# Performance work log

Hardware: AMD Instinct MI355X
Metric: run time of the kernel (lower is better)

The kernel has to match this reference:

```python
import jax, jax.numpy as jnp
import numpy as np

N_NODES = 50000


def gcn_conv(x, W, b, src, dst, n_nodes):
    # PyG GCNConv: h = W x; out = D^{-1/2} (A + I) D^{-1/2} h + b
    h = x @ W  # [N, out_dim]
    ones = jnp.ones(src.shape[0], dtype=x.dtype)
    # degree with self-loops, counted on destination nodes
    deg = jax.ops.segment_sum(ones, dst, num_segments=n_nodes) + 1.0
    dinv = jax.lax.rsqrt(deg)  # deg >= 1, always safe
    norm = dinv[src] * dinv[dst]  # [E]
    agg = jax.ops.segment_sum(h[src] * norm[:, None], dst, num_segments=n_nodes)
    agg = agg + h * (dinv * dinv)[:, None]  # self-loop contribution
    return agg + b


def setup_inputs() -> dict:
    key = jax.random.key(0)
    k1, k2, k3, k4 = jax.random.split(key, 4)
    input_dim, hidden_dim, output_dim = 512, 256, 64
    n_edges = 1_600_000
    x = jax.random.normal(k1, (N_NODES, input_dim), dtype=jnp.float32)
    edge_index = jax.random.randint(k2, (2, n_edges), 0, N_NODES, dtype=jnp.int32)
    W1 = jax.random.normal(k3, (input_dim, hidden_dim), dtype=jnp.float32) / np.sqrt(input_dim)
    b1 = jnp.zeros((hidden_dim,), dtype=jnp.float32)
    W2 = jax.random.normal(k4, (hidden_dim, output_dim), dtype=jnp.float32) / np.sqrt(hidden_dim)
    b2 = jnp.zeros((output_dim,), dtype=jnp.float32)
    return {"x": x, "W1": W1, "b1": b1, "W2": W2, "b2": b2, "edge_index": edge_index}


def reference(x, W1, b1, W2, b2, edge_index):
    src, dst = edge_index[0], edge_index[1]
    h = jax.nn.relu(gcn_conv(x, W1, b1, src, dst, N_NODES))
    h = gcn_conv(h, W2, b2, src, dst, N_NODES)
    return jax.nn.log_softmax(h, axis=1)
```

## Files before the change

kernel.cpp:

```cpp
#include <hip/hip_runtime.h>

#define NODES 50000
#define NBIN 196
#define EPB 2048

typedef __attribute__((ext_vector_type(8))) short short8;
typedef __attribute__((ext_vector_type(4))) float f32x4;
typedef __attribute__((ext_vector_type(2))) float f32x2;

__device__ __forceinline__ ushort f2bf(float f) {
    uint u = __float_as_uint(f);
    uint r = (u + 0x7fffu + ((u >> 16) & 1u)) >> 16;
    return (ushort)r;
}
__device__ __forceinline__ float bf2f(ushort u) {
    return __uint_as_float(((uint)u) << 16);
}
__device__ __forceinline__ uchar f2fp8(float f) {
    return (uchar)(__builtin_amdgcn_cvt_pk_fp8_f32(f, f, 0, false) & 0xff);
}
__device__ __forceinline__ uint cvtpk_bf16(float lo, float hi) {
    uint r;
    asm("v_cvt_pk_bf16_f32 %0, %1, %2" : "=v"(r) : "v"(lo), "v"(hi));
    return r;
}


__global__ __launch_bounds__(256) void k_hist(const int* __restrict__ dst, int E,
                                              int* __restrict__ hist, int nblk) {
    __shared__ int h[NBIN];
    int t = threadIdx.x;
    for (int i = t; i < NBIN; i += 256) h[i] = 0;
    __syncthreads();
    int base = blockIdx.x * EPB;
#pragma unroll
    for (int i = 0; i < EPB / 256; ++i) {
        int e = base + i * 256 + t;
        if (e < E) atomicAdd(&h[dst[e] >> 8], 1);
    }
    __syncthreads();
    for (int i = t; i < NBIN; i += 256) hist[i * nblk + blockIdx.x] = h[i];
}

__global__ __launch_bounds__(1024) void k_scanbin(const int* __restrict__ hist,
                                                  int* __restrict__ offl,
                                                  int* __restrict__ btot, int nblk) {
    __shared__ int s[1024];
    int b = blockIdx.x, t = threadIdx.x;
    int v = (t < nblk) ? hist[b * nblk + t] : 0;
    s[t] = v;
    __syncthreads();
    for (int off = 1; off < 1024; off <<= 1) {
        int u = (t >= off) ? s[t - off] : 0;
        __syncthreads();
        s[t] += u;
        __syncthreads();
    }
    if (t < nblk) offl[b * nblk + t] = s[t] - v;
    if (t == 1023) btot[b] = s[1023];
}

__global__ __launch_bounds__(256) void k_scanoff(const int* __restrict__ btot,
                                                 int* __restrict__ binoff,
                                                 int* __restrict__ rowstart, int E) {
    __shared__ int s[256];
    int t = threadIdx.x;
    int v = (t < NBIN) ? btot[t] : 0;
    s[t] = v;
    __syncthreads();
    for (int off = 1; off < 256; off <<= 1) {
        int u = (t >= off) ? s[t - off] : 0;
        __syncthreads();
        s[t] += u;
        __syncthreads();
    }
    if (t < NBIN) binoff[t] = s[t] - v;
    if (t == 0) { binoff[NBIN] = E; rowstart[NODES] = E; }
}

__global__ __launch_bounds__(256) void k_part(const int* __restrict__ src,
                                              const int* __restrict__ dst, int E,
                                              const int* __restrict__ offl,
                                              const int* __restrict__ binoff, int nblk,
                                              int2* __restrict__ tmp) {
    __shared__ int cur[NBIN];
    int t = threadIdx.x, blk = blockIdx.x;
    for (int i = t; i < NBIN; i += 256) cur[i] = binoff[i] + offl[i * nblk + blk];
    __syncthreads();
    int base = blk * EPB;
#pragma unroll
    for (int i = 0; i < EPB / 256; ++i) {
        int e = base + i * 256 + t;
        if (e < E) {
            int d = dst[e];
            int p = atomicAdd(&cur[d >> 8], 1);
            tmp[p] = make_int2(src[e], d);
        }
    }
}

__global__ __launch_bounds__(256) void k_csr(const int2* __restrict__ tmp,
                                             const int* __restrict__ binoff,
                                             int* __restrict__ rowstart,
                                             float* __restrict__ dinv,
                                             int* __restrict__ esrc) {
    __shared__ int ncnt[256], nst[256];
    int b = blockIdx.x, t = threadIdx.x;
    int e0 = binoff[b], e1 = binoff[b + 1];
    int nb0 = b << 8;
    int nn = min(256, NODES - nb0);
    ncnt[t] = 0;
    __syncthreads();
    for (int e = e0 + t; e < e1; e += 256) atomicAdd(&ncnt[tmp[e].y - nb0], 1);
    __syncthreads();
    int v = ncnt[t];
    nst[t] = v;
    __syncthreads();
    for (int off = 1; off < 256; off <<= 1) {
        int u = (t >= off) ? nst[t - off] : 0;
        __syncthreads();
        nst[t] += u;
        __syncthreads();
    }
    int excl = nst[t] - v;
    if (t < nn) {
        rowstart[nb0 + t] = e0 + excl;
        dinv[nb0 + t] = rsqrtf(1.0f + (float)v);
    }
    __syncthreads();
    ncnt[t] = e0 + excl;
    __syncthreads();
    for (int e = e0 + t; e < e1; e += 256) {
        int2 q = tmp[e];
        int p = atomicAdd(&ncnt[q.y - nb0], 1);
        esrc[p] = q.x;
    }
}

__global__ void k_wfill(const int* __restrict__ esrc, const float* __restrict__ dinv,
                        float* __restrict__ ew, int E) {
    int e = blockIdx.x * blockDim.x + threadIdx.x;
    if (e < E) ew[e] = dinv[esrc[e]];
}


__global__ void k_castT(const float* __restrict__ in, ushort* __restrict__ out, int R, int C) {
    int i = blockIdx.x * blockDim.x + threadIdx.x;
    if (i >= R * C) return;
    int r = i / C, c = i % C;
    out[(size_t)c * R + r] = f2bf(in[i]);
}

__global__ __launch_bounds__(256) void k_gemm1(const float* __restrict__ x,
                                               const ushort* __restrict__ w1t,
                                               uchar* __restrict__ h1f8, int M, int K) {
    constexpr int BM = 64, BN = 128, BK = 64;
    __shared__ __align__(16) ushort As[BM * BK];
    __shared__ __align__(16) ushort Bs[BN * BK];

    int t = threadIdx.x;
    int w = t >> 6, l = t & 63;
    int wm = w & 1, wn = w >> 1;
    int bm = blockIdx.x * BM, bn = blockIdx.y * BN;
    int lr = l & 15, g4 = l >> 4;

    f32x4 acc[2][4] = {};

    int ar = t >> 2;
    int aq = t & 3;
    int arow_g = bm + ar;
    bool aok = arow_g < M;
    const float* ap = x + (size_t)arow_g * K + aq * 16;
    char* adst = (char*)As + ar * 128;
    int aswz = (ar & 7) << 4;

    int brow_loc = l >> 3;
    int bseg = ((l & 7) << 4) ^ (brow_loc << 4);

    for (int k0 = 0; k0 < K; k0 += BK) {
#pragma unroll
        for (int i = 0; i < 4; ++i) {
            int rbase = w * 32 + i * 8;
            const char* gsrc = (const char*)w1t + (size_t)(bn + rbase + brow_loc) * (K * 2) + k0 * 2 + bseg;
            __builtin_amdgcn_global_load_lds(
                (const __attribute__((address_space(1))) uint*)gsrc,
                (__attribute__((address_space(3))) uint*)((char*)Bs + rbase * 128),
                16, 0, 0);
        }
        {
            float4 f[4];
#pragma unroll
            for (int j = 0; j < 4; ++j)
                f[j] = aok ? *(const float4*)(ap + k0 + j * 4) : make_float4(0.f, 0.f, 0.f, 0.f);
#pragma unroll
            for (int j = 0; j < 2; ++j) {
                uint p0 = cvtpk_bf16(f[2 * j].x, f[2 * j].y);
                uint p1 = cvtpk_bf16(f[2 * j].z, f[2 * j].w);
                uint p2 = cvtpk_bf16(f[2 * j + 1].x, f[2 * j + 1].y);
                uint p3 = cvtpk_bf16(f[2 * j + 1].z, f[2 * j + 1].w);
                int4 v = make_int4((int)p0, (int)p1, (int)p2, (int)p3);
                *(int4*)(adst + ((aq * 32 + j * 16) ^ aswz)) = v;
            }
        }
        __syncthreads();
#pragma unroll
        for (int ks = 0; ks < 2; ++ks) {
            short8 af[2], bfr[4];
#pragma unroll
            for (int mt = 0; mt < 2; ++mt) {
                int r = wm * 32 + mt * 16 + lr;
                af[mt] = *(const short8*)((const char*)As + r * 128 + ((ks * 64 + g4 * 16) ^ ((r & 7) << 4)));
            }
#pragma unroll
            for (int nt = 0; nt < 4; ++nt) {
                int r = wn * 64 + nt * 16 + lr;
                bfr[nt] = *(const short8*)((const char*)Bs + r * 128 + ((ks * 64 + g4 * 16) ^ ((r & 7) << 4)));
            }
#pragma unroll
            for (int mt = 0; mt < 2; ++mt)
#pragma unroll
                for (int nt = 0; nt < 4; ++nt)
                    acc[mt][nt] = __builtin_amdgcn_mfma_f32_16x16x32_bf16(af[mt], bfr[nt], acc[mt][nt], 0, 0, 0);
        }
        __syncthreads();
    }

#pragma unroll
    for (int mt = 0; mt < 2; ++mt)
#pragma unroll
        for (int nt = 0; nt < 4; ++nt)
#pragma unroll
            for (int i = 0; i < 4; ++i) {
                int row = bm + wm * 32 + mt * 16 + g4 * 4 + i;
                int col = bn + wn * 64 + nt * 16 + lr;
                if (row < M) h1f8[(size_t)row * 256 + col] = f2fp8(acc[mt][nt][i]);
            }
}

__global__ __launch_bounds__(256) void k_gemm2(const ushort* __restrict__ A,
                                               const ushort* __restrict__ Bt,
                                               ushort* __restrict__ Cb,
                                               int M, int K) {
    constexpr int BM = 64, BN = 64;
    constexpr int NT = 4;
    constexpr int SA = 40;
    __shared__ ushort As[BM * SA];
    __shared__ ushort Bs[BN * SA];

    int t = threadIdx.x;
    int w = t >> 6, l = t & 63;
    int bm = blockIdx.x * BM;
    int lr = l & 15, lk = (l >> 4) * 8;

    f32x4 acc[NT] = {};
    const int ACH = BM * 4;
    const int BCH = BN * 4;

    for (int k0 = 0; k0 < K; k0 += 32) {
        for (int c = t; c < ACH + BCH; c += 256) {
            if (c < ACH) {
                int row = c >> 2, seg = c & 3;
                int gr = bm + row;
                int4 v = make_int4(0, 0, 0, 0);
                if (gr < M) v = *(const int4*)(A + (size_t)gr * K + k0 + seg * 8);
                *(int4*)(&As[row * SA + seg * 8]) = v;
            } else {
                int cc = c - ACH;
                int row = cc >> 2, seg = cc & 3;
                int4 v = *(const int4*)(Bt + (size_t)row * K + k0 + seg * 8);
                *(int4*)(&Bs[row * SA + seg * 8]) = v;
            }
        }
        __syncthreads();
        short8 af = *(const short8*)(&As[(w * 16 + lr) * SA + lk]);
        short8 bfr[NT];
#pragma unroll
        for (int nt = 0; nt < NT; ++nt)
            bfr[nt] = *(const short8*)(&Bs[(nt * 16 + lr) * SA + lk]);
#pragma unroll
        for (int nt = 0; nt < NT; ++nt)
            acc[nt] = __builtin_amdgcn_mfma_f32_16x16x32_bf16(af, bfr[nt], acc[nt], 0, 0, 0);
        __syncthreads();
    }

#pragma unroll
    for (int nt = 0; nt < NT; ++nt)
#pragma unroll
        for (int i = 0; i < 4; ++i) {
            int row = bm + w * 16 + (l >> 4) * 4 + i;
            int col = nt * 16 + lr;
            if (row < M) Cb[(size_t)row * BN + col] = f2bf(acc[nt][i]);
        }
}

__global__ __launch_bounds__(256) void k_agg1(const uchar* __restrict__ h8,
                                              const int* __restrict__ rowstart,
                                              const int* __restrict__ esrc,
                                              const float* __restrict__ ew,
                                              const float* __restrict__ dinv,
                                              const float* __restrict__ b1,
                                              ushort* __restrict__ out) {
    int wave = threadIdx.x >> 6;
    int lane = threadIdx.x & 63;
    int n = blockIdx.x * 4 + wave;
    if (n >= NODES) return;
    float4 acc = make_float4(0.f, 0.f, 0.f, 0.f);
    int e0 = rowstart[n], e1 = rowstart[n + 1];
    int e = e0;
#define A1_STEP(wt, qv)                                                       \
    {                                                                         \
        f32x2 lo = __builtin_amdgcn_cvt_pk_f32_fp8((int)(qv), false);         \
        f32x2 hi = __builtin_amdgcn_cvt_pk_f32_fp8((int)(qv), true);          \
        acc.x = fmaf(wt, lo[0], acc.x);                                       \
        acc.y = fmaf(wt, lo[1], acc.y);                                       \
        acc.z = fmaf(wt, hi[0], acc.z);                                       \
        acc.w = fmaf(wt, hi[1], acc.w);                                       \
    }
    for (; e + 8 <= e1; e += 8) {
        int s0 = esrc[e],     s1 = esrc[e + 1], s2 = esrc[e + 2], s3 = esrc[e + 3];
        int s4 = esrc[e + 4], s5 = esrc[e + 5], s6 = esrc[e + 6], s7 = esrc[e + 7];
        float w0 = ew[e],     w1 = ew[e + 1], w2 = ew[e + 2], w3 = ew[e + 3];
        float w4 = ew[e + 4], w5 = ew[e + 5], w6 = ew[e + 6], w7 = ew[e + 7];
        uint v0 = *(const uint*)(h8 + (size_t)s0 * 256 + lane * 4);
        uint v1 = *(const uint*)(h8 + (size_t)s1 * 256 + lane * 4);
        uint v2 = *(const uint*)(h8 + (size_t)s2 * 256 + lane * 4);
        uint v3 = *(const uint*)(h8 + (size_t)s3 * 256 + lane * 4);
        uint v4 = *(const uint*)(h8 + (size_t)s4 * 256 + lane * 4);
        uint v5 = *(const uint*)(h8 + (size_t)s5 * 256 + lane * 4);
        uint v6 = *(const uint*)(h8 + (size_t)s6 * 256 + lane * 4);
        uint v7 = *(const uint*)(h8 + (size_t)s7 * 256 + lane * 4);
        A1_STEP(w0, v0) A1_STEP(w1, v1) A1_STEP(w2, v2) A1_STEP(w3, v3)
        A1_STEP(w4, v4) A1_STEP(w5, v5) A1_STEP(w6, v6) A1_STEP(w7, v7)
    }
    for (; e < e1; ++e) {
        int s = esrc[e];
        float wt = ew[e];
        uint v = *(const uint*)(h8 + (size_t)s * 256 + lane * 4);
        A1_STEP(wt, v)
    }
#undef A1_STEP
    float dn = dinv[n];
    float s2v = dn * dn;
    uint qs = *(const uint*)(h8 + (size_t)n * 256 + lane * 4);
    f32x2 slo = __builtin_amdgcn_cvt_pk_f32_fp8((int)qs, false);
    f32x2 shi = __builtin_amdgcn_cvt_pk_f32_fp8((int)qs, true);
    float4 bb = *(const float4*)(b1 + lane * 4);
    ushort4 r;
    r.x = f2bf(fmaxf(fmaf(acc.x, dn, fmaf(slo[0], s2v, bb.x)), 0.f));
    r.y = f2bf(fmaxf(fmaf(acc.y, dn, fmaf(slo[1], s2v, bb.y)), 0.f));
    r.z = f2bf(fmaxf(fmaf(acc.z, dn, fmaf(shi[0], s2v, bb.z)), 0.f));
    r.w = f2bf(fmaxf(fmaf(acc.w, dn, fmaf(shi[1], s2v, bb.w)), 0.f));
    *(ushort4*)(out + (size_t)n * 256 + lane * 4) = r;
}

__global__ __launch_bounds__(256) void k_agg2(const ushort* __restrict__ h,
                                              const int* __restrict__ rowstart,
                                              const int* __restrict__ esrc,
                                              const float* __restrict__ ew,
                                              const float* __restrict__ dinv,
                                              const float* __restrict__ b2,
                                              float* __restrict__ out) {
    int wave = threadIdx.x >> 6;
    int lane = threadIdx.x & 63;
    int n = blockIdx.x * 4 + wave;
    if (n >= NODES) return;
    float acc = 0.f;
    int e0 = rowstart[n], e1 = rowstart[n + 1];
    int e = e0;
    for (; e + 8 <= e1; e += 8) {
        int s0 = esrc[e],     s1 = esrc[e + 1], s2 = esrc[e + 2], s3 = esrc[e + 3];
        int s4 = esrc[e + 4], s5 = esrc[e + 5], s6 = esrc[e + 6], s7 = esrc[e + 7];
        float w0 = ew[e],     w1 = ew[e + 1], w2 = ew[e + 2], w3 = ew[e + 3];
        float w4 = ew[e + 4], w5 = ew[e + 5], w6 = ew[e + 6], w7 = ew[e + 7];
        float v0 = bf2f(h[(size_t)s0 * 64 + lane]);
        float v1 = bf2f(h[(size_t)s1 * 64 + lane]);
        float v2 = bf2f(h[(size_t)s2 * 64 + lane]);
        float v3 = bf2f(h[(size_t)s3 * 64 + lane]);
        float v4 = bf2f(h[(size_t)s4 * 64 + lane]);
        float v5 = bf2f(h[(size_t)s5 * 64 + lane]);
        float v6 = bf2f(h[(size_t)s6 * 64 + lane]);
        float v7 = bf2f(h[(size_t)s7 * 64 + lane]);
        acc = fmaf(w0, v0, acc); acc = fmaf(w1, v1, acc);
        acc = fmaf(w2, v2, acc); acc = fmaf(w3, v3, acc);
        acc = fmaf(w4, v4, acc); acc = fmaf(w5, v5, acc);
        acc = fmaf(w6, v6, acc); acc = fmaf(w7, v7, acc);
    }
    for (; e < e1; ++e)
        acc = fmaf(ew[e], bf2f(h[(size_t)esrc[e] * 64 + lane]), acc);
    float dn = dinv[n];
    float r = fmaf(acc, dn, fmaf(bf2f(h[(size_t)n * 64 + lane]), dn * dn, b2[lane]));
    float m = r;
#pragma unroll
    for (int off = 32; off; off >>= 1) m = fmaxf(m, __shfl_xor(m, off));
    float ex = __expf(r - m);
    float ssum = ex;
#pragma unroll
    for (int off = 32; off; off >>= 1) ssum += __shfl_xor(ssum, off);
    out[(size_t)n * 64 + lane] = r - m - __logf(ssum);
}


extern "C" void kernel_launch(void* const* d_in, const int* in_sizes, int n_in,
                              void* d_out, int out_size, void* d_ws, size_t ws_size,
                              hipStream_t stream) {
    const float* x  = (const float*)d_in[0];
    const float* W1 = (const float*)d_in[1];
    const float* b1 = (const float*)d_in[2];
    const float* W2 = (const float*)d_in[3];
    const float* b2 = (const float*)d_in[4];
    const int*   ei = (const int*)d_in[5];
    int E = in_sizes[5] / 2;
    const int* src = ei;
    const int* dst = ei + E;
    float* out = (float*)d_out;

    int nblk = (E + EPB - 1) / EPB;

    char* wsp = (char*)d_ws;
    auto alloc = [&](size_t bytes) {
        char* p = wsp;
        wsp += (bytes + 255) & ~(size_t)255;
        return p;
    };
    int*    hist     = (int*)alloc((size_t)NBIN * nblk * 4);
    int*    offl     = (int*)alloc((size_t)NBIN * nblk * 4);
    int*    btot     = (int*)alloc((size_t)NBIN * 4);
    int*    binoff   = (int*)alloc((size_t)(NBIN + 1) * 4);
    int*    rowstart = (int*)alloc((size_t)(NODES + 1) * 4);
    float*  dinv     = (float*)alloc((size_t)NODES * 4);
    int2*   tmp      = (int2*)alloc((size_t)E * 8);
    int*    esrc     = (int*)alloc((size_t)E * 4);
    float*  ew       = (float*)alloc((size_t)E * 4);
    ushort* w1t      = (ushort*)alloc((size_t)256 * 512 * 2);
    ushort* w2t      = (ushort*)alloc((size_t)64 * 256 * 2);
    uchar*  h1f8     = (uchar*)alloc((size_t)NODES * 256);
    ushort* h1ab     = (ushort*)alloc((size_t)NODES * 256 * 2);
    ushort* h2b      = (ushort*)alloc((size_t)NODES * 64 * 2);

    k_hist<<<nblk, 256, 0, stream>>>(dst, E, hist, nblk);
    k_scanbin<<<NBIN, 1024, 0, stream>>>(hist, offl, btot, nblk);
    k_scanoff<<<1, 256, 0, stream>>>(btot, binoff, rowstart, E);
    k_part<<<nblk, 256, 0, stream>>>(src, dst, E, offl, binoff, nblk, tmp);
    k_csr<<<NBIN, 256, 0, stream>>>(tmp, binoff, rowstart, dinv, esrc);
    k_wfill<<<(E + 255) / 256, 256, 0, stream>>>(esrc, dinv, ew, E);

    k_castT<<<(512 * 256 + 255) / 256, 256, 0, stream>>>(W1, w1t, 512, 256);
    k_castT<<<(256 * 64 + 255) / 256, 256, 0, stream>>>(W2, w2t, 256, 64);

    k_gemm1<<<dim3((NODES + 63) / 64, 2), 256, 0, stream>>>(x, w1t, h1f8, NODES, 512);
    k_agg1<<<(NODES + 3) / 4, 256, 0, stream>>>(h1f8, rowstart, esrc, ew, dinv, b1, h1ab);

    k_gemm2<<<(NODES + 63) / 64, 256, 0, stream>>>(h1ab, w2t, h2b, NODES, 256);
    k_agg2<<<(NODES + 3) / 4, 256, 0, stream>>>(h2b, rowstart, esrc, ew, dinv, b2, out);
}
```

Baseline: 226.3 us.

## Fuse edge partition into GEMM1 launch and scalarize aggregation row bounds

Merges the edge-partition kernel into the first GEMM launch as extra blocks in the same grid, so the memory-bound scatter can overlap with the compute-bound GEMM and one launch is removed. The GEMM grid is flattened to 1D, with the N tile taken from the low bit of the block index. In both aggregation kernels, the wave index and row bounds are forced into scalar registers via readfirstlane, and the per-lane base pointer is hoisted out of the loop. The fused kernel's shared-memory footprint covers both roles, which may slightly lower occupancy, and the partition blocks are scheduled after the GEMM blocks.

```diff
diff --git a/kernel.cpp b/kernel.cpp
--- a/kernel.cpp
+++ b/kernel.cpp
@@ -76,27 +76,6 @@
     }
     if (t < NBIN) binoff[t] = s[t] - v;
     if (t == 0) { binoff[NBIN] = E; rowstart[NODES] = E; }
-}
-
-__global__ __launch_bounds__(256) void k_part(const int* __restrict__ src,
-                                              const int* __restrict__ dst, int E,
-                                              const int* __restrict__ offl,
-                                              const int* __restrict__ binoff, int nblk,
-                                              int2* __restrict__ tmp) {
-    __shared__ int cur[NBIN];
-    int t = threadIdx.x, blk = blockIdx.x;
-    for (int i = t; i < NBIN; i += 256) cur[i] = binoff[i] + offl[i * nblk + blk];
-    __syncthreads();
-    int base = blk * EPB;
-#pragma unroll
-    for (int i = 0; i < EPB / 256; ++i) {
-        int e = base + i * 256 + t;
-        if (e < E) {
-            int d = dst[e];
-            int p = atomicAdd(&cur[d >> 8], 1);
-            tmp[p] = make_int2(src[e], d);
-        }
-    }
 }
 
 __global__ __launch_bounds__(256) void k_csr(const int2* __restrict__ tmp,
@@ -151,17 +130,40 @@
     out[(size_t)c * R + r] = f2bf(in[i]);
 }
 
-__global__ __launch_bounds__(256) void k_gemm1(const float* __restrict__ x,
-                                               const ushort* __restrict__ w1t,
-                                               uchar* __restrict__ h1f8, int M, int K) {
+__global__ __launch_bounds__(256) void k_gemm1_part(
+    const float* __restrict__ x, const ushort* __restrict__ w1t,
+    uchar* __restrict__ h1f8, int M, int K,
+    const int* __restrict__ src, const int* __restrict__ dst, int E,
+    const int* __restrict__ offl, const int* __restrict__ binoff, int nblk,
+    int2* __restrict__ tmp, int gemmBlocks) {
     constexpr int BM = 64, BN = 128, BK = 64;
     __shared__ __align__(16) ushort As[BM * BK];
     __shared__ __align__(16) ushort Bs[BN * BK];
+    __shared__ int cur[NBIN];
 
     int t = threadIdx.x;
+
+    if (blockIdx.x >= gemmBlocks) {
+        int blk = blockIdx.x - gemmBlocks;
+        for (int i = t; i < NBIN; i += 256) cur[i] = binoff[i] + offl[i * nblk + blk];
+        __syncthreads();
+        int base = blk * EPB;
+#pragma unroll
+        for (int i = 0; i < EPB / 256; ++i) {
+            int e = base + i * 256 + t;
+            if (e < E) {
+                int d = dst[e];
+                int p = atomicAdd(&cur[d >> 8], 1);
+                tmp[p] = make_int2(src[e], d);
+            }
+        }
+        return;
+    }
+
     int w = t >> 6, l = t & 63;
     int wm = w & 1, wn = w >> 1;
-    int bm = blockIdx.x * BM, bn = blockIdx.y * BN;
+    int bm = (blockIdx.x >> 1) * BM;
+    int bn = (blockIdx.x & 1) * BN;
     int lr = l & 15, g4 = l >> 4;
 
     f32x4 acc[2][4] = {};
@@ -300,12 +302,14 @@
                                               const float* __restrict__ dinv,
                                               const float* __restrict__ b1,
                                               ushort* __restrict__ out) {
-    int wave = threadIdx.x >> 6;
+    int wave = __builtin_amdgcn_readfirstlane(threadIdx.x >> 6);
     int lane = threadIdx.x & 63;
     int n = blockIdx.x * 4 + wave;
     if (n >= NODES) return;
+    const uchar* hl = h8 + lane * 4;
     float4 acc = make_float4(0.f, 0.f, 0.f, 0.f);
-    int e0 = rowstart[n], e1 = rowstart[n + 1];
+    int e0 = __builtin_amdgcn_readfirstlane(rowstart[n]);
+    int e1 = __builtin_amdgcn_readfirstlane(rowstart[n + 1]);
     int e = e0;
 #define A1_STEP(wt, qv)                                                       \
     {                                                                         \
@@ -321,27 +325,27 @@
         int s4 = esrc[e + 4], s5 = esrc[e + 5], s6 = esrc[e + 6], s7 = esrc[e + 7];
         float w0 = ew[e],     w1 = ew[e + 1], w2 = ew[e + 2], w3 = ew[e + 3];
         float w4 = ew[e + 4], w5 = ew[e + 5], w6 = ew[e + 6], w7 = ew[e + 7];
-        uint v0 = *(const uint*)(h8 + (size_t)s0 * 256 + lane * 4);
-        uint v1 = *(const uint*)(h8 + (size_t)s1 * 256 + lane * 4);
-        uint v2 = *(const uint*)(h8 + (size_t)s2 * 256 + lane * 4);
-        uint v3 = *(const uint*)(h8 + (size_t)s3 * 256 + lane * 4);
-        uint v4 = *(const uint*)(h8 + (size_t)s4 * 256 + lane * 4);
-        uint v5 = *(const uint*)(h8 + (size_t)s5 * 256 + lane * 4);
-        uint v6 = *(const uint*)(h8 + (size_t)s6 * 256 + lane * 4);
-        uint v7 = *(const uint*)(h8 + (size_t)s7 * 256 + lane * 4);
+        uint v0 = *(const uint*)(hl + (size_t)s0 * 256);
+        uint v1 = *(const uint*)(hl + (size_t)s1 * 256);
+        uint v2 = *(const uint*)(hl + (size_t)s2 * 256);
+        uint v3 = *(const uint*)(hl + (size_t)s3 * 256);
+        uint v4 = *(const uint*)(hl + (size_t)s4 * 256);
+        uint v5 = *(const uint*)(hl + (size_t)s5 * 256);
+        uint v6 = *(const uint*)(hl + (size_t)s6 * 256);
+        uint v7 = *(const uint*)(hl + (size_t)s7 * 256);
         A1_STEP(w0, v0) A1_STEP(w1, v1) A1_STEP(w2, v2) A1_STEP(w3, v3)
         A1_STEP(w4, v4) A1_STEP(w5, v5) A1_STEP(w6, v6) A1_STEP(w7, v7)
     }
     for (; e < e1; ++e) {
         int s = esrc[e];
         float wt = ew[e];
-        uint v = *(const uint*)(h8 + (size_t)s * 256 + lane * 4);
+        uint v = *(const uint*)(hl + (size_t)s * 256);
         A1_STEP(wt, v)
     }
 #undef A1_STEP
     float dn = dinv[n];
     float s2v = dn * dn;
-    uint qs = *(const uint*)(h8 + (size_t)n * 256 + lane * 4);
+    uint qs = *(const uint*)(hl + (size_t)n * 256);
     f32x2 slo = __builtin_amdgcn_cvt_pk_f32_fp8((int)qs, false);
     f32x2 shi = __builtin_amdgcn_cvt_pk_f32_fp8((int)qs, true);
     float4 bb = *(const float4*)(b1 + lane * 4);
@@ -360,35 +364,37 @@
                                               const float* __restrict__ dinv,
                                               const float* __restrict__ b2,
                                               float* __restrict__ out) {
-    int wave = threadIdx.x >> 6;
+    int wave = __builtin_amdgcn_readfirstlane(threadIdx.x >> 6);
     int lane = threadIdx.x & 63;
     int n = blockIdx.x * 4 + wave;
     if (n >= NODES) return;
+    const ushort* hl = h + lane;
     float acc = 0.f;
-    int e0 = rowstart[n], e1 = rowstart[n + 1];
+    int e0 = __builtin_amdgcn_readfirstlane(rowstart[n]);
+    int e1 = __builtin_amdgcn_readfirstlane(rowstart[n + 1]);
     int e = e0;
     for (; e + 8 <= e1; e += 8) {
         int s0 = esrc[e],     s1 = esrc[e + 1], s2 = esrc[e + 2], s3 = esrc[e + 3];
         int s4 = esrc[e + 4], s5 = esrc[e + 5], s6 = esrc[e + 6], s7 = esrc[e + 7];
         float w0 = ew[e],     w1 = ew[e + 1], w2 = ew[e + 2], w3 = ew[e + 3];
         float w4 = ew[e + 4], w5 = ew[e + 5], w6 = ew[e + 6], w7 = ew[e + 7];
-        float v0 = bf2f(h[(size_t)s0 * 64 + lane]);
-        float v1 = bf2f(h[(size_t)s1 * 64 + lane]);
-        float v2 = bf2f(h[(size_t)s2 * 64 + lane]);
-        float v3 = bf2f(h[(size_t)s3 * 64 + lane]);
-        float v4 = bf2f(h[(size_t)s4 * 64 + lane]);
-        float v5 = bf2f(h[(size_t)s5 * 64 + lane]);
-        float v6 = bf2f(h[(size_t)s6 * 64 + lane]);
-        float v7 = bf2f(h[(size_t)s7 * 64 + lane]);
+        float v0 = bf2f(hl[(size_t)s0 * 64]);
+        float v1 = bf2f(hl[(size_t)s1 * 64]);
+        float v2 = bf2f(hl[(size_t)s2 * 64]);
+        float v3 = bf2f(hl[(size_t)s3 * 64]);
+        float v4 = bf2f(hl[(size_t)s4 * 64]);
+        float v5 = bf2f(hl[(size_t)s5 * 64]);
+        float v6 = bf2f(hl[(size_t)s6 * 64]);
+        float v7 = bf2f(hl[(size_t)s7 * 64]);
         acc = fmaf(w0, v0, acc); acc = fmaf(w1, v1, acc);
         acc = fmaf(w2, v2, acc); acc = fmaf(w3, v3, acc);
         acc = fmaf(w4, v4, acc); acc = fmaf(w5, v5, acc);
         acc = fmaf(w6, v6, acc); acc = fmaf(w7, v7, acc);
     }
     for (; e < e1; ++e)
-        acc = fmaf(ew[e], bf2f(h[(size_t)esrc[e] * 64 + lane]), acc);
+        acc = fmaf(ew[e], bf2f(hl[(size_t)esrc[e] * 64]), acc);
     float dn = dinv[n];
-    float r = fmaf(acc, dn, fmaf(bf2f(h[(size_t)n * 64 + lane]), dn * dn, b2[lane]));
+    float r = fmaf(acc, dn, fmaf(bf2f(hl[(size_t)n * 64]), dn * dn, b2[lane]));
     float m = r;
 #pragma unroll
     for (int off = 32; off; off >>= 1) m = fmaxf(m, __shfl_xor(m, off));
@@ -440,14 +446,18 @@
     k_hist<<<nblk, 256, 0, stream>>>(dst, E, hist, nblk);
     k_scanbin<<<NBIN, 1024, 0, stream>>>(hist, offl, btot, nblk);
     k_scanoff<<<1, 256, 0, stream>>>(btot, binoff, rowstart, E);
-    k_part<<<nblk, 256, 0, stream>>>(src, dst, E, offl, binoff, nblk, tmp);
+
+    k_castT<<<(512 * 256 + 255) / 256, 256, 0, stream>>>(W1, w1t, 512, 256);
+    k_castT<<<(256 * 64 + 255) / 256, 256, 0, stream>>>(W2, w2t, 256, 64);
+
+    int gemmBlocks = ((NODES + 63) / 64) * 2;
+    k_gemm1_part<<<gemmBlocks + nblk, 256, 0, stream>>>(
+        x, w1t, h1f8, NODES, 512,
+        src, dst, E, offl, binoff, nblk, tmp, gemmBlocks);
+
     k_csr<<<NBIN, 256, 0, stream>>>(tmp, binoff, rowstart, dinv, esrc);
     k_wfill<<<(E + 255) / 256, 256, 0, stream>>>(esrc, dinv, ew, E);
 
-    k_castT<<<(512 * 256 + 255) / 256, 256, 0, stream>>>(W1, w1t, 512, 256);
-    k_castT<<<(256 * 64 + 255) / 256, 256, 0, stream>>>(W2, w2t, 256, 64);
-
-    k_gemm1<<<dim3((NODES + 63) / 64, 2), 256, 0, stream>>>(x, w1t, h1f8, NODES, 512);
     k_agg1<<<(NODES + 3) / 4, 256, 0, stream>>>(h1f8, rowstart, esrc, ew, dinv, b1, h1ab);
 
     k_gemm2<<<(NODES + 63) / 64, 256, 0, stream>>>(h1ab, w2t, h2b, NODES, 256);
```

After: 200.9 us. 11.2% less time.

## Pack 16-bit source index and bf16 edge weight into one word per edge

Applied to the files above, without the earlier changes.

Each edge's source index (16 bits, since node ids fit below 65536) and its bf16 normalisation weight now share one 32-bit word, so both aggregation kernels read one stream instead of separate int index and float weight arrays. The CSR partition buffer is also shrunk to 4 bytes per edge by keeping only the low byte of the destination. Separately, the gemm1 grid is flattened so the two N tiles of the same row block run next to each other, which should help L2 reuse of x, and per-wave values are made scalar with readfirstlane. In exchange, edge weights are rounded to bf16 and the code assumes fewer than 65536 nodes.

```diff
diff --git a/kernel.cpp b/kernel.cpp
--- a/kernel.cpp
+++ b/kernel.cpp
@@ -82,7 +82,7 @@
                                               const int* __restrict__ dst, int E,
                                               const int* __restrict__ offl,
                                               const int* __restrict__ binoff, int nblk,
-                                              int2* __restrict__ tmp) {
+                                              uint* __restrict__ tmp) {
     __shared__ int cur[NBIN];
     int t = threadIdx.x, blk = blockIdx.x;
     for (int i = t; i < NBIN; i += 256) cur[i] = binoff[i] + offl[i * nblk + blk];
@@ -94,16 +94,16 @@
         if (e < E) {
             int d = dst[e];
             int p = atomicAdd(&cur[d >> 8], 1);
-            tmp[p] = make_int2(src[e], d);
-        }
-    }
-}
-
-__global__ __launch_bounds__(256) void k_csr(const int2* __restrict__ tmp,
+            tmp[p] = (uint)src[e] | ((uint)(d & 0xff) << 16);
+        }
+    }
+}
+
+__global__ __launch_bounds__(256) void k_csr(const uint* __restrict__ tmp,
                                              const int* __restrict__ binoff,
                                              int* __restrict__ rowstart,
                                              float* __restrict__ dinv,
-                                             int* __restrict__ esrc) {
+                                             ushort* __restrict__ esrc16) {
     __shared__ int ncnt[256], nst[256];
     int b = blockIdx.x, t = threadIdx.x;
     int e0 = binoff[b], e1 = binoff[b + 1];
@@ -111,7 +111,7 @@
     int nn = min(256, NODES - nb0);
     ncnt[t] = 0;
     __syncthreads();
-    for (int e = e0 + t; e < e1; e += 256) atomicAdd(&ncnt[tmp[e].y - nb0], 1);
+    for (int e = e0 + t; e < e1; e += 256) atomicAdd(&ncnt[(tmp[e] >> 16) & 0xff], 1);
     __syncthreads();
     int v = ncnt[t];
     nst[t] = v;
@@ -131,16 +131,19 @@
     ncnt[t] = e0 + excl;
     __syncthreads();
     for (int e = e0 + t; e < e1; e += 256) {
-        int2 q = tmp[e];
-        int p = atomicAdd(&ncnt[q.y - nb0], 1);
-        esrc[p] = q.x;
-    }
-}
-
-__global__ void k_wfill(const int* __restrict__ esrc, const float* __restrict__ dinv,
-                        float* __restrict__ ew, int E) {
+        uint q = tmp[e];
+        int p = atomicAdd(&ncnt[(q >> 16) & 0xff], 1);
+        esrc16[p] = (ushort)(q & 0xffff);
+    }
+}
+
+__global__ void k_wfill(const ushort* __restrict__ esrc16, const float* __restrict__ dinv,
+                        uint* __restrict__ epack, int E) {
     int e = blockIdx.x * blockDim.x + threadIdx.x;
-    if (e < E) ew[e] = dinv[esrc[e]];
+    if (e < E) {
+        int s = esrc16[e];
+        epack[e] = (uint)s | ((uint)f2bf(dinv[s]) << 16);
+    }
 }
 
 
@@ -161,7 +164,8 @@
     int t = threadIdx.x;
     int w = t >> 6, l = t & 63;
     int wm = w & 1, wn = w >> 1;
-    int bm = blockIdx.x * BM, bn = blockIdx.y * BN;
+    int bm = (blockIdx.x >> 1) * BM;
+    int bn = (blockIdx.x & 1) * BN;
     int lr = l & 15, g4 = l >> 4;
 
     f32x4 acc[2][4] = {};
@@ -295,20 +299,22 @@
 
 __global__ __launch_bounds__(256) void k_agg1(const uchar* __restrict__ h8,
                                               const int* __restrict__ rowstart,
-                                              const int* __restrict__ esrc,
-                                              const float* __restrict__ ew,
+                                              const uint* __restrict__ ep,
                                               const float* __restrict__ dinv,
                                               const float* __restrict__ b1,
                                               ushort* __restrict__ out) {
-    int wave = threadIdx.x >> 6;
+    int wave = __builtin_amdgcn_readfirstlane(threadIdx.x >> 6);
     int lane = threadIdx.x & 63;
     int n = blockIdx.x * 4 + wave;
     if (n >= NODES) return;
+    const uchar* hl = h8 + lane * 4;
     float4 acc = make_float4(0.f, 0.f, 0.f, 0.f);
-    int e0 = rowstart[n], e1 = rowstart[n + 1];
+    int e0 = __builtin_amdgcn_readfirstlane(rowstart[n]);
+    int e1 = __builtin_amdgcn_readfirstlane(rowstart[n + 1]);
     int e = e0;
-#define A1_STEP(wt, qv)                                                       \
+#define A1_STEP(q, qv)                                                        \
     {                                                                         \
+        float wt = bf2f((ushort)((q) >> 16));                                 \
         f32x2 lo = __builtin_amdgcn_cvt_pk_f32_fp8((int)(qv), false);         \
         f32x2 hi = __builtin_amdgcn_cvt_pk_f32_fp8((int)(qv), true);          \
         acc.x = fmaf(wt, lo[0], acc.x);                                       \
@@ -317,31 +323,28 @@
         acc.w = fmaf(wt, hi[1], acc.w);                                       \
     }
     for (; e + 8 <= e1; e += 8) {
-        int s0 = esrc[e],     s1 = esrc[e + 1], s2 = esrc[e + 2], s3 = esrc[e + 3];
-        int s4 = esrc[e + 4], s5 = esrc[e + 5], s6 = esrc[e + 6], s7 = esrc[e + 7];
-        float w0 = ew[e],     w1 = ew[e + 1], w2 = ew[e + 2], w3 = ew[e + 3];
-        float w4 = ew[e + 4], w5 = ew[e + 5], w6 = ew[e + 6], w7 = ew[e + 7];
-        uint v0 = *(const uint*)(h8 + (size_t)s0 * 256 + lane * 4);
-        uint v1 = *(const uint*)(h8 + (size_t)s1 * 256 + lane * 4);
-        uint v2 = *(const uint*)(h8 + (size_t)s2 * 256 + lane * 4);
-        uint v3 = *(const uint*)(h8 + (size_t)s3 * 256 + lane * 4);
-        uint v4 = *(const uint*)(h8 + (size_t)s4 * 256 + lane * 4);
-        uint v5 = *(const uint*)(h8 + (size_t)s5 * 256 + lane * 4);
-        uint v6 = *(const uint*)(h8 + (size_t)s6 * 256 + lane * 4);
-        uint v7 = *(const uint*)(h8 + (size_t)s7 * 256 + lane * 4);
-        A1_STEP(w0, v0) A1_STEP(w1, v1) A1_STEP(w2, v2) A1_STEP(w3, v3)
-        A1_STEP(w4, v4) A1_STEP(w5, v5) A1_STEP(w6, v6) A1_STEP(w7, v7)
+        uint q0 = ep[e],     q1 = ep[e + 1], q2 = ep[e + 2], q3 = ep[e + 3];
+        uint q4 = ep[e + 4], q5 = ep[e + 5], q6 = ep[e + 6], q7 = ep[e + 7];
+        uint v0 = *(const uint*)(hl + (size_t)(q0 & 0xffff) * 256);
+        uint v1 = *(const uint*)(hl + (size_t)(q1 & 0xffff) * 256);
+        uint v2 = *(const uint*)(hl + (size_t)(q2 & 0xffff) * 256);
+        uint v3 = *(const uint*)(hl + (size_t)(q3 & 0xffff) * 256);
+        uint v4 = *(const uint*)(hl + (size_t)(q4 & 0xffff) * 256);
+        uint v5 = *(const uint*)(hl + (size_t)(q5 & 0xffff) * 256);
+        uint v6 = *(const uint*)(hl + (size_t)(q6 & 0xffff) * 256);
+        uint v7 = *(const uint*)(hl + (size_t)(q7 & 0xffff) * 256);
+        A1_STEP(q0, v0) A1_STEP(q1, v1) A1_STEP(q2, v2) A1_STEP(q3, v3)
+        A1_STEP(q4, v4) A1_STEP(q5, v5) A1_STEP(q6, v6) A1_STEP(q7, v7)
     }
     for (; e < e1; ++e) {
-        int s = esrc[e];
-        float wt = ew[e];
-        uint v = *(const uint*)(h8 + (size_t)s * 256 + lane * 4);
-        A1_STEP(wt, v)
+        uint q = ep[e];
+        uint v = *(const uint*)(hl + (size_t)(q & 0xffff) * 256);
+        A1_STEP(q, v)
     }
 #undef A1_STEP
     float dn = dinv[n];
     float s2v = dn * dn;
-    uint qs = *(const uint*)(h8 + (size_t)n * 256 + lane * 4);
+    uint qs = *(const uint*)(hl + (size_t)n * 256);
     f32x2 slo = __builtin_amdgcn_cvt_pk_f32_fp8((int)qs, false);
     f32x2 shi = __builtin_amdgcn_cvt_pk_f32_fp8((int)qs, true);
     float4 bb = *(const float4*)(b1 + lane * 4);
@@ -355,40 +358,45 @@
 
 __global__ __launch_bounds__(256) void k_agg2(const ushort* __restrict__ h,
                                               const int* __restrict__ rowstart,
-                                              const int* __restrict__ esrc,
-                                              const float* __restrict__ ew,
+                                              const uint* __restrict__ ep,
                                               const float* __restrict__ dinv,
                                               const float* __restrict__ b2,
                                               float* __restrict__ out) {
-    int wave = threadIdx.x >> 6;
+    int wave = __builtin_amdgcn_readfirstlane(threadIdx.x >> 6);
     int lane = threadIdx.x & 63;
     int n = blockIdx.x * 4 + wave;
     if (n >= NODES) return;
+    const ushort* hl = h + lane;
     float acc = 0.f;
-    int e0 = rowstart[n], e1 = rowstart[n + 1];
+    int e0 = __builtin_amdgcn_readfirstlane(rowstart[n]);
+    int e1 = __builtin_amdgcn_readfirstlane(rowstart[n + 1]);
     int e = e0;
     for (; e + 8 <= e1; e += 8) {
-        int s0 = esrc[e],     s1 = esrc[e + 1], s2 = esrc[e + 2], s3 = esrc[e + 3];
-        int s4 = esrc[e + 4], s5 = esrc[e + 5], s6 = esrc[e + 6], s7 = esrc[e + 7];
-        float w0 = ew[e],     w1 = ew[e + 1], w2 = ew[e + 2], w3 = ew[e + 3];
-        float w4 = ew[e + 4], w5 = ew[e + 5], w6 = ew[e + 6], w7 = ew[e + 7];
-        float v0 = bf2f(h[(size_t)s0 * 64 + lane]);
-        float v1 = bf2f(h[(size_t)s1 * 64 + lane]);
-        float v2 = bf2f(h[(size_t)s2 * 64 + lane]);
-        float v3 = bf2f(h[(size_t)s3 * 64 + lane]);
-        float v4 = bf2f(h[(size_t)s4 * 64 + lane]);
-        float v5 = bf2f(h[(size_t)s5 * 64 + lane]);
-        float v6 = bf2f(h[(size_t)s6 * 64 + lane]);
-        float v7 = bf2f(h[(size_t)s7 * 64 + lane]);
-        acc = fmaf(w0, v0, acc); acc = fmaf(w1, v1, acc);
-        acc = fmaf(w2, v2, acc); acc = fmaf(w3, v3, acc);
-        acc = fmaf(w4, v4, acc); acc = fmaf(w5, v5, acc);
-        acc = fmaf(w6, v6, acc); acc = fmaf(w7, v7, acc);
-    }
-    for (; e < e1; ++e)
-        acc = fmaf(ew[e], bf2f(h[(size_t)esrc[e] * 64 + lane]), acc);
+        uint q0 = ep[e],     q1 = ep[e + 1], q2 = ep[e + 2], q3 = ep[e + 3];
+        uint q4 = ep[e + 4], q5 = ep[e + 5], q6 = ep[e + 6], q7 = ep[e + 7];
+        float v0 = bf2f(hl[(size_t)(q0 & 0xffff) * 64]);
+        float v1 = bf2f(hl[(size_t)(q1 & 0xffff) * 64]);
+        float v2 = bf2f(hl[(size_t)(q2 & 0xffff) * 64]);
+        float v3 = bf2f(hl[(size_t)(q3 & 0xffff) * 64]);
+        float v4 = bf2f(hl[(size_t)(q4 & 0xffff) * 64]);
+        float v5 = bf2f(hl[(size_t)(q5 & 0xffff) * 64]);
+        float v6 = bf2f(hl[(size_t)(q6 & 0xffff) * 64]);
+        float v7 = bf2f(hl[(size_t)(q7 & 0xffff) * 64]);
+        acc = fmaf(bf2f((ushort)(q0 >> 16)), v0, acc);
+        acc = fmaf(bf2f((ushort)(q1 >> 16)), v1, acc);
+        acc = fmaf(bf2f((ushort)(q2 >> 16)), v2, acc);
+        acc = fmaf(bf2f((ushort)(q3 >> 16)), v3, acc);
+        acc = fmaf(bf2f((ushort)(q4 >> 16)), v4, acc);
+        acc = fmaf(bf2f((ushort)(q5 >> 16)), v5, acc);
+        acc = fmaf(bf2f((ushort)(q6 >> 16)), v6, acc);
+        acc = fmaf(bf2f((ushort)(q7 >> 16)), v7, acc);
+    }
+    for (; e < e1; ++e) {
+        uint q = ep[e];
+        acc = fmaf(bf2f((ushort)(q >> 16)), bf2f(hl[(size_t)(q & 0xffff) * 64]), acc);
+    }
     float dn = dinv[n];
-    float r = fmaf(acc, dn, fmaf(bf2f(h[(size_t)n * 64 + lane]), dn * dn, b2[lane]));
+    float r = fmaf(acc, dn, fmaf(bf2f(hl[(size_t)n * 64]), dn * dn, b2[lane]));
     float m = r;
 #pragma unroll
     for (int off = 32; off; off >>= 1) m = fmaxf(m, __shfl_xor(m, off));
@@ -428,9 +436,9 @@
     int*    binoff   = (int*)alloc((size_t)(NBIN + 1) * 4);
     int*    rowstart = (int*)alloc((size_t)(NODES + 1) * 4);
     float*  dinv     = (float*)alloc((size_t)NODES * 4);
-    int2*   tmp      = (int2*)alloc((size_t)E * 8);
-    int*    esrc     = (int*)alloc((size_t)E * 4);
-    float*  ew       = (float*)alloc((size_t)E * 4);
+    uint*   tmp      = (uint*)alloc((size_t)E * 4);
+    ushort* esrc16   = (ushort*)alloc((size_t)E * 2);
+    uint*   epack    = (uint*)alloc((size_t)E * 4);
     ushort* w1t      = (ushort*)alloc((size_t)256 * 512 * 2);
     ushort* w2t      = (ushort*)alloc((size_t)64 * 256 * 2);
     uchar*  h1f8     = (uchar*)alloc((size_t)NODES * 256);
@@ -441,15 +449,15 @@
     k_scanbin<<<NBIN, 1024, 0, stream>>>(hist, offl, btot, nblk);
     k_scanoff<<<1, 256, 0, stream>>>(btot, binoff, rowstart, E);
     k_part<<<nblk, 256, 0, stream>>>(src, dst, E, offl, binoff, nblk, tmp);
-    k_csr<<<NBIN, 256, 0, stream>>>(tmp, binoff, rowstart, dinv, esrc);
-    k_wfill<<<(E + 255) / 256, 256, 0, stream>>>(esrc, dinv, ew, E);
+    k_csr<<<NBIN, 256, 0, stream>>>(tmp, binoff, rowstart, dinv, esrc16);
+    k_wfill<<<(E + 255) / 256, 256, 0, stream>>>(esrc16, dinv, epack, E);
 
     k_castT<<<(512 * 256 + 255) / 256, 256, 0, stream>>>(W1, w1t, 512, 256);
     k_castT<<<(256 * 64 + 255) / 256, 256, 0, stream>>>(W2, w2t, 256, 64);
 
-    k_gemm1<<<dim3((NODES + 63) / 64, 2), 256, 0, stream>>>(x, w1t, h1f8, NODES, 512);
-    k_agg1<<<(NODES + 3) / 4, 256, 0, stream>>>(h1f8, rowstart, esrc, ew, dinv, b1, h1ab);
+    k_gemm1<<<((NODES + 63) / 64) * 2, 256, 0, stream>>>(x, w1t, h1f8, NODES, 512);
+    k_agg1<<<(NODES + 3) / 4, 256, 0, stream>>>(h1f8, rowstart, epack, dinv, b1, h1ab);
 
     k_gemm2<<<(NODES + 63) / 64, 256, 0, stream>>>(h1ab, w2t, h2b, NODES, 256);
-    k_agg2<<<(NODES + 3) / 4, 256, 0, stream>>>(h2b, rowstart, esrc, ew, dinv, b2, out);
-}
+    k_agg2<<<(NODES + 3) / 4, 256, 0, stream>>>(h2b, rowstart, epack, dinv, b2, out);
+}
```

After: 200.4 us. 11.4% less time.
